# Kernel tuning notes

Hardware: AMD Instinct MI355X
Metric: run time of the kernel (lower is better)

The kernel has to match this reference:

```python
import jax, jax.numpy as jnp
import numpy as np

K = 20
NEG_SLOPE = 0.2
BN_EPS = 1e-5


def knn_idx(x, k):
    # x: (B, C, N) -> neighbor indices (B, N, k) by largest negative sq-distance
    xt = jnp.swapaxes(x, 1, 2)                      # (B, N, C)
    inner = 2.0 * jnp.einsum('bic,bjc->bij', xt, xt)
    sq = jnp.sum(xt * xt, axis=-1)                  # (B, N)
    dist = inner - sq[:, :, None] - sq[:, None, :]  # -||xi-xj||^2
    _, idx = jax.lax.top_k(dist, k)
    return idx


def edge_feature(x, src, idx):
    # x: (B, C, N) centers; src: (B, C, M) gather source; idx: (B, N, k)
    xt = jnp.swapaxes(x, 1, 2)                      # (B, N, C)
    st = jnp.swapaxes(src, 1, 2)                    # (B, M, C)
    b = jnp.arange(xt.shape[0])[:, None, None]
    neigh = st[b, idx]                              # (B, N, k, C)
    center = xt[:, :, None, :]                      # (B, N, 1, C)
    feat = jnp.concatenate(
        [neigh - center, jnp.broadcast_to(center, neigh.shape)], axis=-1)
    return jnp.transpose(feat, (0, 3, 1, 2))        # (B, 2C, N, k)


def conv_bn_lrelu(x, w, gamma, beta):
    # 1x1 conv (no bias) + training-mode BatchNorm2d + LeakyReLU(0.2)
    y = jnp.einsum('oc,bcnk->bonk', w, x)
    mean = jnp.mean(y, axis=(0, 2, 3), keepdims=True)
    var = jnp.var(y, axis=(0, 2, 3), keepdims=True)
    y = (y - mean) * jax.lax.rsqrt(var + BN_EPS)
    y = y * gamma[None, :, None, None] + beta[None, :, None, None]
    return jnp.where(y >= 0, y, NEG_SLOPE * y)


def knn_ia_idx(x, y, k):
    # cosine-similarity KNN from x (B,Cx,N) into y (B,Cy,M), normalize over channels
    xn = x / jnp.maximum(jnp.linalg.norm(x, axis=1, keepdims=True), 1e-12)
    yn = y / jnp.maximum(jnp.linalg.norm(y, axis=1, keepdims=True), 1e-12)
    simi = jnp.einsum('bci,bcj->bij', xn, yn)       # (B, N, M)
    _, idx = jax.lax.top_k(simi, k)
    return idx


def setup_inputs() -> dict:
    key = jax.random.key(0)
    ks = jax.random.split(key, 8)
    B, N, M, EMB = 8, 1024, 1024, 512
    x = jax.random.normal(ks[0], (B, 3, N), dtype=jnp.float32)
    y = jax.random.normal(ks[1], (B, 128, M), dtype=jnp.float32)
    def w(k_, o, c):
        return jax.random.normal(k_, (o, c), dtype=jnp.float32) * (1.0 / np.sqrt(c))
    inp = {
        'x': x, 'y': y,
        'w1': w(ks[2], 64, 6),
        'w2': w(ks[3], 64, 128),
        'w3': w(ks[4], 128, 128),
        'w4': w(ks[5], 256, 256),
        'w5': w(ks[6], EMB, 512),
        'g1': jnp.ones(64), 'b1': jnp.zeros(64),
        'g2': jnp.ones(64), 'b2': jnp.zeros(64),
        'g3': jnp.ones(128), 'b3': jnp.zeros(128),
        'g4': jnp.ones(256), 'b4': jnp.zeros(256),
        'g5': jnp.ones(EMB), 'b5': jnp.zeros(EMB),
    }
    return inp


def reference(x, y, w1, w2, w3, w4, w5, g1, b1, g2, b2, g3, b3, g4, b4, g5, b5):
    # block 1
    h = conv_bn_lrelu(edge_feature(x, x, knn_idx(x, K)), w1, g1, b1)
    x1 = jnp.max(h, axis=-1)                        # (B, 64, N)
    # block 2
    h = conv_bn_lrelu(edge_feature(x1, x1, knn_idx(x1, K)), w2, g2, b2)
    x2 = jnp.max(h, axis=-1)                        # (B, 64, N)
    # block 3
    h = conv_bn_lrelu(edge_feature(x2, x2, knn_idx(x2, K)), w3, g3, b3)
    x3 = jnp.max(h, axis=-1)                        # (B, 128, N)
    # block 4: cross-attention KNN into y (cosine similarity)
    h = conv_bn_lrelu(edge_feature(x3, y, knn_ia_idx(x3, y, K)), w4, g4, b4)
    x4 = jnp.max(h, axis=-1)                        # (B, 256, N)
    # final 1x1 conv + BN + LeakyReLU on concatenated features (512 ch)
    cat = jnp.concatenate([x1, x2, x3, x4], axis=1)  # (B, 512, N)
    out = conv_bn_lrelu(cat[..., None], w5, g5, b5)[..., 0]
    return out                                       # (B, n_emb_dims, N)
```

## Files before the change

kernel.cpp:

```cpp
#include <hip/hip_runtime.h>
#include <hip/hip_bf16.h>

#define KNN 20
#define NEG_SLOPE 0.2f

constexpr int BB = 8;
constexpr int NN = 1024;
constexpr int MM = 1024;

typedef short bf16x8 __attribute__((ext_vector_type(8)));
typedef float f32x4 __attribute__((ext_vector_type(4)));

__device__ __forceinline__ void topk_exact_f64(double (&v)[16], int lane, int* op) {
  for (int r = 0; r < KNN; ++r) {
    double bv = -INFINITY;
    int bj = MM;
#pragma unroll
    for (int m = 0; m < 16; ++m) {
      if (v[m] > bv) { bv = v[m]; bj = m * 64 + lane; }
    }
#pragma unroll
    for (int off = 32; off > 0; off >>= 1) {
      double ov = __shfl_xor(bv, off, 64);
      int oj = __shfl_xor(bj, off, 64);
      if (ov > bv || (ov == bv && oj < bj)) { bv = ov; bj = oj; }
    }
    if (bj < MM && lane == (bj & 63)) v[bj >> 6] = -INFINITY;
    if (lane == 0) op[r] = bj;
  }
}

__device__ __forceinline__ void topk20(double (&v)[16], int lane, int* op) {
  unsigned s[16];
#pragma unroll
  for (int m = 0; m < 16; ++m) {
    float f = (float)v[m];
    unsigned u = __float_as_uint(f);
    u = (u & 0x80000000u) ? ~u : (u | 0x80000000u);
    s[m] = (u & ~1023u) | (unsigned)(1023 - (m * 64 + lane));
  }
#pragma unroll
  for (int p = 1; p < 16; p <<= 1) {
#pragma unroll
    for (int k = p; k >= 1; k >>= 1) {
#pragma unroll
      for (int j = k % p; j + k < 16; j += 2 * k) {
#pragma unroll
        for (int i = 0; i < k; ++i) {
          int a = j + i, b = j + i + k;
          if (b < 16 && (a / (2 * p)) == (b / (2 * p))) {
            unsigned hi = s[a] > s[b] ? s[a] : s[b];
            unsigned lo = s[a] > s[b] ? s[b] : s[a];
            s[a] = hi;
            s[b] = lo;
          }
        }
      }
    }
  }
  unsigned prev = 0;
#pragma unroll
  for (int r = 0; r < KNN; ++r) {
    unsigned win = s[0];
#pragma unroll
    for (int off = 32; off > 0; off >>= 1) {
      unsigned o = __shfl_xor(win, off, 64);
      win = o > win ? o : win;
    }
    if (lane == 0) op[r] = 1023 - (int)(win & 1023u);
    if (s[0] == win) {
#pragma unroll
      for (int i = 0; i < 15; ++i) s[i] = s[i + 1];
      s[15] = 0u;
    }
    prev = win;
  }
  unsigned win21 = s[0];
#pragma unroll
  for (int off = 32; off > 0; off >>= 1) {
    unsigned o = __shfl_xor(win21, off, 64);
    win21 = o > win21 ? o : win21;
  }
  if ((prev >> 10) == (win21 >> 10)) {
    topk_exact_f64(v, lane, op);
  }
}

__global__ __launch_bounds__(256) void k_transpose(
    const float* __restrict__ in, float* __restrict__ out, int C, int Np) {
  int total = BB * C * Np;
  for (int t = blockIdx.x * 256 + threadIdx.x; t < total; t += gridDim.x * 256) {
    int c = t % C;
    int n = (t / C) % Np;
    int b = t / (C * Np);
    out[t] = in[((size_t)b * C + c) * Np + n];
  }
}

__global__ __launch_bounds__(256) void k_cvt_bf16(
    const float* __restrict__ in, __hip_bfloat16* __restrict__ out, int n) {
  int i = blockIdx.x * 256 + threadIdx.x;
  if (i < n) out[i] = __float2bfloat16(in[i]);
}

template <int RECIP>
__global__ __launch_bounds__(256) void k_rowsq(
    const float* __restrict__ A, int ld, int C, double* __restrict__ sq) {
  int p = blockIdx.x * 256 + threadIdx.x;
  if (p >= BB * NN) return;
  const float* row = A + (size_t)p * ld;
  double s = 0.0;
  for (int c = 0; c < C; ++c) { double v = (double)row[c]; s += v * v; }
  if (RECIP) {
    sq[p] = 1.0 / fmax(sqrt(s), 1e-12);
  } else {
    sq[p] = s;
  }
}

__global__ __launch_bounds__(256) void k_knn3(
    const float* __restrict__ xs3, const double* __restrict__ sq, int* __restrict__ idx) {
  __shared__ float P[NN * 3];
  int b = blockIdx.x;
  const float* Xb = xs3 + (size_t)b * NN * 3;
  int tid = threadIdx.x;
  for (int t = tid; t < NN * 3; t += 256) P[t] = Xb[t];
  __syncthreads();
  int wave = tid >> 6, lane = tid & 63;
  int i = blockIdx.y * 4 + wave;
  double xi = (double)P[i * 3], yi = (double)P[i * 3 + 1], zi = (double)P[i * 3 + 2];
  double sqi = sq[b * NN + i];
  double v[16];
#pragma unroll
  for (int m = 0; m < 16; ++m) {
    int j = m * 64 + lane;
    double d = fma(xi, (double)P[j * 3], 0.0);
    d = fma(yi, (double)P[j * 3 + 1], d);
    d = fma(zi, (double)P[j * 3 + 2], d);
    v[m] = 2.0 * d - sqi - sq[b * NN + j];
  }
  int* op = idx + ((size_t)b * NN + i) * KNN;
  topk20(v, lane, op);
}

template <int MODE>
__global__ __launch_bounds__(256) void k_gram2(
    const float* __restrict__ A, int lda, const float* __restrict__ Bm, int ldb,
    const double* __restrict__ sqA, const double* __restrict__ sqB,
    double* __restrict__ D, int C, int b0) {
  __shared__ double As[16][136];
  __shared__ double Bs[16][72];
  int bg = b0 + blockIdx.x;
  int bl = blockIdx.x;
  int j0 = blockIdx.y * 64;
  int i0 = blockIdx.z * 128;
  const float* Ab = A + (size_t)bg * NN * lda;
  const float* Bb = Bm + (size_t)bg * MM * ldb;
  int tx = threadIdx.x, ty = threadIdx.y;
  int tid = ty * 16 + tx;
  double acc[8][4] = {};
  for (int c0 = 0; c0 < C; c0 += 16) {
    for (int r = 0; r < 2; ++r) {
      int li = tid + r * 256;
      int row = li >> 2;
      int f = (li & 3) * 4;
      float4 av = *(const float4*)&Ab[(size_t)(i0 + row) * lda + c0 + f];
      As[f + 0][row] = (double)av.x;
      As[f + 1][row] = (double)av.y;
      As[f + 2][row] = (double)av.z;
      As[f + 3][row] = (double)av.w;
    }
    {
      int row = tid >> 2;
      int f = (tid & 3) * 4;
      float4 bv = *(const float4*)&Bb[(size_t)(j0 + row) * ldb + c0 + f];
      Bs[f + 0][row] = (double)bv.x;
      Bs[f + 1][row] = (double)bv.y;
      Bs[f + 2][row] = (double)bv.z;
      Bs[f + 3][row] = (double)bv.w;
    }
    __syncthreads();
#pragma unroll
    for (int k = 0; k < 16; ++k) {
      double a_[8], b_[4];
#pragma unroll
      for (int ii = 0; ii < 8; ++ii) a_[ii] = As[k][ty * 8 + ii];
#pragma unroll
      for (int jj = 0; jj < 4; ++jj) b_[jj] = Bs[k][jj * 16 + tx];
#pragma unroll
      for (int ii = 0; ii < 8; ++ii)
#pragma unroll
        for (int jj = 0; jj < 4; ++jj)
          acc[ii][jj] = fma(a_[ii], b_[jj], acc[ii][jj]);
    }
    __syncthreads();
  }
  for (int ii = 0; ii < 8; ++ii) {
    int i = i0 + ty * 8 + ii;
    for (int jj = 0; jj < 4; ++jj) {
      int j = j0 + jj * 16 + tx;
      double r = acc[ii][jj];
      if (MODE == 1) r = 2.0 * r - sqA[bg * NN + i] - sqB[bg * NN + j];
      if (MODE == 2) r = r * sqA[bg * NN + i] * sqB[bg * NN + j];
      D[((size_t)bl * NN + i) * MM + j] = r;
    }
  }
}

__global__ __launch_bounds__(256) void k_gram_sym(
    const float* __restrict__ A, int lda, const double* __restrict__ sqA,
    double* __restrict__ D, int C, int b0) {
  __shared__ double As[16][68];
  __shared__ double Bs[16][68];
  __shared__ double T[64][65];
  int p = blockIdx.y;
  int r = (int)((sqrtf(8.f * p + 1.f) - 1.f) * 0.5f);
  while ((r + 1) * (r + 2) / 2 <= p) ++r;
  while (r * (r + 1) / 2 > p) --r;
  int cc = p - r * (r + 1) / 2;
  int i0 = r * 64, j0 = cc * 64;
  int bg = b0 + blockIdx.x;
  int bl = blockIdx.x;
  const float* Ab = A + (size_t)bg * NN * lda;
  int tx = threadIdx.x, ty = threadIdx.y;
  int tid = ty * 16 + tx;
  double acc[4][4] = {};
  for (int c0 = 0; c0 < C; c0 += 16) {
    for (int rr = 0; rr < 4; ++rr) {
      int li = tid + rr * 256;
      int row = li >> 4, k = li & 15;
      int c = c0 + k;
      As[k][row] = (c < C) ? (double)Ab[(size_t)(i0 + row) * lda + c] : 0.0;
      Bs[k][row] = (c < C) ? (double)Ab[(size_t)(j0 + row) * lda + c] : 0.0;
    }
    __syncthreads();
#pragma unroll
    for (int k = 0; k < 16; ++k) {
      double a_[4], b_[4];
#pragma unroll
      for (int ii = 0; ii < 4; ++ii) a_[ii] = As[k][ty * 4 + ii];
#pragma unroll
      for (int jj = 0; jj < 4; ++jj) b_[jj] = Bs[k][jj * 16 + tx];
#pragma unroll
      for (int ii = 0; ii < 4; ++ii)
#pragma unroll
        for (int jj = 0; jj < 4; ++jj)
          acc[ii][jj] = fma(a_[ii], b_[jj], acc[ii][jj]);
    }
    __syncthreads();
  }
  for (int ii = 0; ii < 4; ++ii) {
    int i = i0 + ty * 4 + ii;
    for (int jj = 0; jj < 4; ++jj) {
      int j = j0 + jj * 16 + tx;
      double v = 2.0 * acc[ii][jj] - sqA[bg * NN + i] - sqA[bg * NN + j];
      D[((size_t)bl * NN + i) * MM + j] = v;
      T[jj * 16 + tx][ty * 4 + ii] = v;
    }
  }
  if (i0 != j0) {
    __syncthreads();
    for (int rr = 0; rr < 16; ++rr) {
      int li = tid + rr * 256;
      int jrow = li >> 6, il = li & 63;
      D[((size_t)bl * NN + j0 + jrow) * MM + i0 + il] = T[jrow][il];
    }
  }
}

__global__ __launch_bounds__(256) void k_topk(const double* __restrict__ D,
                                              int* __restrict__ idx, int b0) {
  int wave = threadIdx.x >> 6;
  int lane = threadIdx.x & 63;
  int bl = blockIdx.x;
  int row = blockIdx.y * 4 + wave;
  const double* rp = D + ((size_t)bl * NN + row) * MM;
  double v[16];
#pragma unroll
  for (int m = 0; m < 16; ++m) v[m] = rp[m * 64 + lane];
  int* op = idx + ((size_t)(b0 + bl) * NN + row) * KNN;
  topk20(v, lane, op);
}

__global__ __launch_bounds__(256) void k_featmm(
    const float* __restrict__ src, int lds_, const float* __restrict__ w, int CW,
    float* __restrict__ out, int C, int O, int mode, int Np) {
  __shared__ float As[16][68];
  __shared__ float Ws[16][68];
  int b = blockIdx.x;
  int o0 = blockIdx.y * 64;
  int j0 = blockIdx.z * 64;
  int tx = threadIdx.x, ty = threadIdx.y;
  int tid = ty * 16 + tx;
  const float* Sb = src + (size_t)b * Np * lds_;
  float acc[4][4] = {};
  for (int c0 = 0; c0 < C; c0 += 16) {
    for (int r = 0; r < 4; ++r) {
      int li = tid + r * 256;
      int row = li >> 4, k = li & 15;
      int c = c0 + k;
      As[k][row] = (c < C) ? Sb[(size_t)(j0 + row) * lds_ + c] : 0.f;
      float wv = 0.f;
      if (c < C) {
        const float* wr = w + (size_t)(o0 + row) * CW;
        wv = mode == 0 ? wr[c] : (wr[C + c] - wr[c]);
      }
      Ws[k][row] = wv;
    }
    __syncthreads();
#pragma unroll
    for (int k = 0; k < 16; ++k) {
      float a_[4], b_[4];
#pragma unroll
      for (int ii = 0; ii < 4; ++ii) a_[ii] = As[k][ty * 4 + ii];
#pragma unroll
      for (int jj = 0; jj < 4; ++jj) b_[jj] = Ws[k][tx * 4 + jj];
#pragma unroll
      for (int ii = 0; ii < 4; ++ii)
#pragma unroll
        for (int jj = 0; jj < 4; ++jj)
          acc[ii][jj] = fmaf(a_[ii], b_[jj], acc[ii][jj]);
    }
    __syncthreads();
  }
  for (int ii = 0; ii < 4; ++ii) {
    int j = j0 + ty * 4 + ii;
    float4 v;
    float* vp = &v.x;
    for (int jj = 0; jj < 4; ++jj) vp[jj] = acc[ii][jj];
    *(float4*)&out[((size_t)b * Np + j) * O + o0 + tx * 4] = v;
  }
}

__global__ __launch_bounds__(256) void k_gemm5_mfma(
    const __hip_bfloat16* __restrict__ cath, const __hip_bfloat16* __restrict__ w5h,
    float* __restrict__ out) {
  int b = blockIdx.x;
  int j0 = blockIdx.y * 16;
  int o0 = blockIdx.z * 64 + (threadIdx.x >> 6) * 16;
  int lane = threadIdx.x & 63;
  int m = lane & 15;
  int quad = lane >> 4;
  const __hip_bfloat16* arow = cath + ((size_t)b * NN + j0 + m) * 512 + quad * 8;
  const __hip_bfloat16* brow = w5h + (size_t)(o0 + m) * 512 + quad * 8;
  f32x4 acc = {0.f, 0.f, 0.f, 0.f};
#pragma unroll
  for (int c0 = 0; c0 < 512; c0 += 32) {
    bf16x8 a = *(const bf16x8*)(arow + c0);
    bf16x8 bb = *(const bf16x8*)(brow + c0);
    acc = __builtin_amdgcn_mfma_f32_16x16x32_bf16(a, bb, acc, 0, 0, 0);
  }
  float* obase = &out[((size_t)b * NN + j0 + quad * 4) * 512 + o0 + m];
#pragma unroll
  for (int r = 0; r < 4; ++r) obase[(size_t)r * 512] = acc[r];
}

__global__ __launch_bounds__(256) void k_gather(
    const float* __restrict__ u, const float* __restrict__ t, const int* __restrict__ idx,
    double* __restrict__ stats, float* __restrict__ mx, int O, int srcNp) {
  __shared__ int lidx[16 * KNN];
  __shared__ double rs[256];
  __shared__ double rq[256];
  int b = blockIdx.x;
  int n0 = blockIdx.y * 16;
  int o0 = blockIdx.z * 64;
  int tid = threadIdx.x;
  int lane = tid & 63, nsl = tid >> 6;
  for (int w = tid; w < 16 * KNN; w += 256)
    lidx[w] = idx[((size_t)b * NN + n0) * KNN + w];
  __syncthreads();
  int oo = o0 + lane;
  double s1 = 0.0, s2 = 0.0;
  for (int ns = nsl; ns < 16; ns += 4) {
    size_t row = (size_t)b * NN + n0 + ns;
    float tv = t[row * O + oo];
    float mxv = -INFINITY, a1 = 0.f, a2 = 0.f;
#pragma unroll
    for (int k = 0; k < KNN; ++k) {
      int j = lidx[ns * KNN + k];
      float yv = u[((size_t)b * srcNp + j) * O + oo] + tv;
      mxv = fmaxf(mxv, yv);
      a1 += yv;
      a2 = fmaf(yv, yv, a2);
    }
    mx[row * O + oo] = mxv;
    s1 += (double)a1;
    s2 += (double)a2;
  }
  rs[tid] = s1;
  rq[tid] = s2;
  __syncthreads();
  if (tid < 64) {
    s1 = rs[tid] + rs[tid + 64] + rs[tid + 128] + rs[tid + 192];
    s2 = rq[tid] + rq[tid + 64] + rq[tid + 128] + rq[tid + 192];
    atomicAdd(&stats[o0 + tid], s1);
    atomicAdd(&stats[O + o0 + tid], s2);
  }
}

__global__ void k_bnfin(const double* __restrict__ stats, const float* __restrict__ gamma,
                        const float* __restrict__ beta, float* __restrict__ sc,
                        int O, double cnt) {
  int o = threadIdx.x;
  if (o >= O) return;
  double mean = stats[o] / cnt;
  double var = stats[O + o] / cnt - mean * mean;
  if (var < 0.0) var = 0.0;
  double rstd = 1.0 / sqrt(var + 1e-5);
  float s = gamma[o] * (float)rstd;
  float c = beta[o] - (float)mean * s;
  sc[o] = s;
  sc[O + o] = c;
}

__global__ __launch_bounds__(256) void k_bnapply(
    const float* __restrict__ mx, const float* __restrict__ u, const float* __restrict__ t,
    const int* __restrict__ idx, const float* __restrict__ sc, float* __restrict__ cat,
    __hip_bfloat16* __restrict__ cath, int coff, int O, int srcNp) {
  int i = blockIdx.x * 256 + threadIdx.x;
  int total = BB * NN * O;
  if (i >= total) return;
  int oo = i % O;
  int n = (i / O) % NN;
  int b = i / (O * NN);
  float s = sc[oo], c = sc[O + oo];
  float v;
  if (s >= 0.f) {
    v = mx[i];
  } else {
    float tv = t[i];
    float mn = INFINITY;
    for (int k = 0; k < KNN; ++k) {
      int j = idx[((size_t)b * NN + n) * KNN + k];
      mn = fminf(mn, u[((size_t)b * srcNp + j) * O + oo] + tv);
    }
    v = mn;
  }
  float a = s * v + c;
  a = (a >= 0.f) ? a : NEG_SLOPE * a;
  size_t oidx = ((size_t)b * NN + n) * 512 + coff + oo;
  cat[oidx] = a;
  cath[oidx] = __float2bfloat16(a);
}

__global__ __launch_bounds__(256) void k_stats512(
    const float* __restrict__ y5, double* __restrict__ stats) {
  int b = blockIdx.y;
  int n0 = blockIdx.x * 32;
  int tid = threadIdx.x;
  for (int part = 0; part < 2; ++part) {
    int oo = tid + part * 256;
    float a1 = 0.f, a2 = 0.f;
    for (int ns = 0; ns < 32; ++ns) {
      float v = y5[((size_t)b * NN + n0 + ns) * 512 + oo];
      a1 += v;
      a2 = fmaf(v, v, a2);
    }
    atomicAdd(&stats[oo], (double)a1);
    atomicAdd(&stats[512 + oo], (double)a2);
  }
}

__global__ __launch_bounds__(256) void k_final5b(
    const float* __restrict__ y5, const float* __restrict__ sc, float* __restrict__ out) {
  __shared__ float tile[64][65];
  int b = blockIdx.z;
  int n0 = blockIdx.x * 64;
  int o0 = blockIdx.y * 64;
  int tid = threadIdx.x;
  for (int r = 0; r < 16; ++r) {
    int li = tid + r * 256;
    int nl = li >> 6, ol = li & 63;
    float v = y5[((size_t)b * NN + n0 + nl) * 512 + o0 + ol];
    float a = sc[o0 + ol] * v + sc[512 + o0 + ol];
    a = (a >= 0.f) ? a : NEG_SLOPE * a;
    tile[nl][ol] = a;
  }
  __syncthreads();
  for (int r = 0; r < 16; ++r) {
    int li = tid + r * 256;
    int ol = li >> 6, nl = li & 63;
    out[((size_t)b * 512 + o0 + ol) * NN + n0 + nl] = tile[nl][ol];
  }
}

__global__ __launch_bounds__(256) void k_mmstats(
    const float* __restrict__ src, const float* __restrict__ w,
    double* __restrict__ stats) {
  __shared__ float As[16][68];
  __shared__ float Ws[16][68];
  __shared__ float redS[16][64];
  __shared__ float redQ[16][64];
  int b = blockIdx.z;
  int j0 = blockIdx.y * 64;
  int o0 = blockIdx.x * 64;
  int tx = threadIdx.x, ty = threadIdx.y;
  int tid = ty * 16 + tx;
  const float* Sb = src + (size_t)b * NN * 512;
  float acc[4][4] = {};
  for (int c0 = 0; c0 < 512; c0 += 16) {
    for (int r = 0; r < 4; ++r) {
      int li = tid + r * 256;
      int row = li >> 4, k = li & 15;
      As[k][row] = Sb[(size_t)(j0 + row) * 512 + c0 + k];
      Ws[k][row] = w[(size_t)(o0 + row) * 512 + c0 + k];
    }
    __syncthreads();
#pragma unroll
    for (int k = 0; k < 16; ++k) {
      float a_[4], b_[4];
#pragma unroll
      for (int ii = 0; ii < 4; ++ii) a_[ii] = As[k][ty * 4 + ii];
#pragma unroll
      for (int jj = 0; jj < 4; ++jj) b_[jj] = Ws[k][tx * 4 + jj];
#pragma unroll
      for (int ii = 0; ii < 4; ++ii)
#pragma unroll
        for (int jj = 0; jj < 4; ++jj)
          acc[ii][jj] = fmaf(a_[ii], b_[jj], acc[ii][jj]);
    }
    __syncthreads();
  }
  for (int jj = 0; jj < 4; ++jj) {
    float s = 0.f, q = 0.f;
    for (int ii = 0; ii < 4; ++ii) { float v = acc[ii][jj]; s += v; q += v * v; }
    redS[ty][tx * 4 + jj] = s;
    redQ[ty][tx * 4 + jj] = q;
  }
  __syncthreads();
  if (tid < 64) {
    float s = 0.f, q = 0.f;
    for (int r = 0; r < 16; ++r) { s += redS[r][tid]; q += redQ[r][tid]; }
    atomicAdd(&stats[o0 + tid], (double)s);
    atomicAdd(&stats[512 + o0 + tid], (double)q);
  }
}

__global__ __launch_bounds__(256) void k_final5(
    const float* __restrict__ src, const float* __restrict__ w,
    const float* __restrict__ sc, float* __restrict__ out) {
  __shared__ float As[16][68];
  __shared__ float Ws[16][68];
  __shared__ float tile[64][65];
  int b = blockIdx.z;
  int j0 = blockIdx.y * 64;
  int o0 = blockIdx.x * 64;
  int tx = threadIdx.x, ty = threadIdx.y;
  int tid = ty * 16 + tx;
  const float* Sb = src + (size_t)b * NN * 512;
  float acc[4][4] = {};
  for (int c0 = 0; c0 < 512; c0 += 16) {
    for (int r = 0; r < 4; ++r) {
      int li = tid + r * 256;
      int row = li >> 4, k = li & 15;
      As[k][row] = Sb[(size_t)(j0 + row) * 512 + c0 + k];
      Ws[k][row] = w[(size_t)(o0 + row) * 512 + c0 + k];
    }
    __syncthreads();
#pragma unroll
    for (int k = 0; k < 16; ++k) {
      float a_[4], b_[4];
#pragma unroll
      for (int ii = 0; ii < 4; ++ii) a_[ii] = As[k][ty * 4 + ii];
#pragma unroll
      for (int jj = 0; jj < 4; ++jj) b_[jj] = Ws[k][tx * 4 + jj];
#pragma unroll
      for (int ii = 0; ii < 4; ++ii)
#pragma unroll
        for (int jj = 0; jj < 4; ++jj)
          acc[ii][jj] = fmaf(a_[ii], b_[jj], acc[ii][jj]);
    }
    __syncthreads();
  }
  for (int ii = 0; ii < 4; ++ii)
    for (int jj = 0; jj < 4; ++jj) {
      int nl = ty * 4 + ii, ol = tx * 4 + jj;
      float a = sc[o0 + ol] * acc[ii][jj] + sc[512 + o0 + ol];
      a = (a >= 0.f) ? a : NEG_SLOPE * a;
      tile[nl][ol] = a;
    }
  __syncthreads();
  for (int r = 0; r < 16; ++r) {
    int li = tid + r * 256;
    int ol = li >> 6, nl = li & 63;
    out[((size_t)b * 512 + o0 + ol) * NN + j0 + nl] = tile[nl][ol];
  }
}

extern "C" void kernel_launch(void* const* d_in, const int* in_sizes, int n_in,
                              void* d_out, int out_size, void* d_ws, size_t ws_size,
                              hipStream_t stream) {
  const float* x = (const float*)d_in[0];
  const float* y = (const float*)d_in[1];
  const float* w1 = (const float*)d_in[2];
  const float* w2 = (const float*)d_in[3];
  const float* w3 = (const float*)d_in[4];
  const float* w4 = (const float*)d_in[5];
  const float* w5 = (const float*)d_in[6];
  const float* g1 = (const float*)d_in[7];
  const float* b1 = (const float*)d_in[8];
  const float* g2 = (const float*)d_in[9];
  const float* b2 = (const float*)d_in[10];
  const float* g3 = (const float*)d_in[11];
  const float* b3 = (const float*)d_in[12];
  const float* g4 = (const float*)d_in[13];
  const float* b4 = (const float*)d_in[14];
  const float* g5 = (const float*)d_in[15];
  const float* b5 = (const float*)d_in[16];

  char* base = (char*)d_ws;
  size_t off = 0;
  auto alloc = [&](size_t bytes) -> char* {
    char* p = base + off;
    off += (bytes + 255) & ~(size_t)255;
    return p;
  };
  double* st = (double*)alloc(1024 * 8);
  float* sc  = (float*)alloc(1024 * 4);
  double* sq  = (double*)alloc((size_t)BB * NN * 8);
  double* rnx = (double*)alloc((size_t)BB * NN * 8);
  double* rny = (double*)alloc((size_t)BB * MM * 8);
  int*   idxb = (int*)alloc((size_t)BB * NN * KNN * 4);
  float* xs3 = (float*)alloc((size_t)BB * NN * 3 * 4);
  float* ys  = (float*)alloc((size_t)BB * MM * 128 * 4);
  float* cat = (float*)alloc((size_t)BB * NN * 512 * 4);
  __hip_bfloat16* cath = (__hip_bfloat16*)alloc((size_t)BB * NN * 512 * 2);
  __hip_bfloat16* w5h  = (__hip_bfloat16*)alloc((size_t)512 * 512 * 2);
  size_t ddBatchBytes = (size_t)NN * MM * 8;
  size_t avail = (ws_size > off) ? (ws_size - off) : 0;
  int CB = (int)(avail / ddBatchBytes);
  if (CB < 1) CB = 1;
  if (CB > BB) CB = BB;
  char*  U   = alloc((size_t)CB * ddBatchBytes);
  double* DD = (double*)U;
  float* tt  = (float*)U;
  float* y5  = (float*)U;
  float* uu  = (float*)d_out;
  float* mx  = (float*)d_out + (size_t)2 * 1024 * 1024;
  float* outp = (float*)d_out;

  const dim3 blk2(16, 16);
  const double cntE = (double)BB * NN * KNN;

  auto knn = [&](const float* A, int lda, const float* Bm, int ldb,
                 const double* sa, const double* sb, int C, int mode, int sym) {
    for (int b0 = 0; b0 < BB; b0 += CB) {
      int cb = (BB - b0 < CB) ? (BB - b0) : CB;
      if (sym) {
        k_gram_sym<<<dim3(cb, 136), blk2, 0, stream>>>(A, lda, sa, DD, C, b0);
      } else {
        dim3 g(cb, MM / 64, NN / 128);
        if (mode == 1) k_gram2<1><<<g, blk2, 0, stream>>>(A, lda, Bm, ldb, sa, sb, DD, C, b0);
        else           k_gram2<2><<<g, blk2, 0, stream>>>(A, lda, Bm, ldb, sa, sb, DD, C, b0);
      }
      k_topk<<<dim3(cb, 256), 256, 0, stream>>>(DD, idxb, b0);
    }
  };

  auto edge_layer = [&](const float* ctr, int ldc, const float* src, int ldsrc, int srcNp,
                        const float* w, int CW, const float* g, const float* bb,
                        int C, int O, int coff) {
    k_featmm<<<dim3(8, O / 64, 16), blk2, 0, stream>>>(src, ldsrc, w, CW, uu, C, O, 0, srcNp);
    k_featmm<<<dim3(8, O / 64, 16), blk2, 0, stream>>>(ctr, ldc, w, CW, tt, C, O, 1, NN);
    hipMemsetAsync(st, 0, 1024 * 8, stream);
    k_gather<<<dim3(BB, NN / 16, O / 64), 256, 0, stream>>>(uu, tt, idxb, st, mx, O, srcNp);
    k_bnfin<<<1, O, 0, stream>>>(st, g, bb, sc, O, cntE);
    k_bnapply<<<(BB * NN * O + 255) / 256, 256, 0, stream>>>(mx, uu, tt, idxb, sc, cat,
                                                             cath, coff, O, srcNp);
  };

  k_transpose<<<96, 256, 0, stream>>>(x, xs3, 3, NN);
  k_transpose<<<2048, 256, 0, stream>>>(y, ys, 128, MM);
  k_cvt_bf16<<<1024, 256, 0, stream>>>(w5, w5h, 512 * 512);

  k_rowsq<0><<<32, 256, 0, stream>>>(xs3, 3, 3, sq);
  k_knn3<<<dim3(BB, 256), 256, 0, stream>>>(xs3, sq, idxb);
  edge_layer(xs3, 3, xs3, 3, NN, w1, 6, g1, b1, 3, 64, 0);

  k_rowsq<0><<<32, 256, 0, stream>>>(cat, 512, 64, sq);
  knn(cat, 512, cat, 512, sq, sq, 64, 1, 1);
  edge_layer(cat, 512, cat, 512, NN, w2, 128, g2, b2, 64, 64, 64);

  k_rowsq<0><<<32, 256, 0, stream>>>(cat + 64, 512, 64, sq);
  knn(cat + 64, 512, cat + 64, 512, sq, sq, 64, 1, 1);
  edge_layer(cat + 64, 512, cat + 64, 512, NN, w3, 128, g3, b3, 64, 128, 128);

  k_rowsq<1><<<32, 256, 0, stream>>>(cat + 128, 512, 128, rnx);
  k_rowsq<1><<<32, 256, 0, stream>>>(ys, 128, 128, rny);
  knn(cat + 128, 512, ys, 128, rnx, rny, 128, 2, 0);
  edge_layer(cat + 128, 512, ys, 128, MM, w4, 256, g4, b4, 128, 256, 256);

  hipMemsetAsync(st, 0, 1024 * 8, stream);
  if (CB >= 2) {
    k_gemm5_mfma<<<dim3(BB, 64, 8), 256, 0, stream>>>(cath, w5h, y5);
    k_stats512<<<dim3(32, 8), 256, 0, stream>>>(y5, st);
    k_bnfin<<<1, 512, 0, stream>>>(st, g5, b5, sc, 512, (double)(BB * NN));
    k_final5b<<<dim3(16, 8, 8), 256, 0, stream>>>(y5, sc, outp);
  } else {
    k_mmstats<<<dim3(8, 16, 8), blk2, 0, stream>>>(cat, w5, st);
    k_bnfin<<<1, 512, 0, stream>>>(st, g5, b5, sc, 512, (double)(BB * NN));
    k_final5<<<dim3(8, 16, 8), blk2, 0, stream>>>(cat, w5, sc, outp);
  }
}
```

Baseline: 694.9 us.

## Emit packed 32-bit top-k keys from gram kernels and merge feature matmuls

```diff
diff --git a/kernel.cpp b/kernel.cpp
--- a/kernel.cpp
+++ b/kernel.cpp
@@ -10,6 +10,13 @@
 
 typedef short bf16x8 __attribute__((ext_vector_type(8)));
 typedef float f32x4 __attribute__((ext_vector_type(4)));
+
+__device__ __forceinline__ unsigned pack_key(double d, int j) {
+  float f = (float)d;
+  unsigned u = __float_as_uint(f);
+  u = (u & 0x80000000u) ? ~u : (u | 0x80000000u);
+  return (u & ~1023u) | (unsigned)(1023 - j);
+}
 
 __device__ __forceinline__ void topk_exact_f64(double (&v)[16], int lane, int* op) {
   for (int r = 0; r < KNN; ++r) {
@@ -30,15 +37,7 @@
   }
 }
 
-__device__ __forceinline__ void topk20(double (&v)[16], int lane, int* op) {
-  unsigned s[16];
-#pragma unroll
-  for (int m = 0; m < 16; ++m) {
-    float f = (float)v[m];
-    unsigned u = __float_as_uint(f);
-    u = (u & 0x80000000u) ? ~u : (u | 0x80000000u);
-    s[m] = (u & ~1023u) | (unsigned)(1023 - (m * 64 + lane));
-  }
+__device__ __forceinline__ bool topk20_fast(unsigned (&s)[16], int lane, int* op) {
 #pragma unroll
   for (int p = 1; p < 16; p <<= 1) {
 #pragma unroll
@@ -81,9 +80,7 @@
     unsigned o = __shfl_xor(win21, off, 64);
     win21 = o > win21 ? o : win21;
   }
-  if ((prev >> 10) == (win21 >> 10)) {
-    topk_exact_f64(v, lane, op);
-  }
+  return (prev >> 10) == (win21 >> 10);
 }
 
 __global__ __launch_bounds__(256) void k_transpose(
@@ -131,6 +128,7 @@
   double xi = (double)P[i * 3], yi = (double)P[i * 3 + 1], zi = (double)P[i * 3 + 2];
   double sqi = sq[b * NN + i];
   double v[16];
+  unsigned s[16];
 #pragma unroll
   for (int m = 0; m < 16; ++m) {
     int j = m * 64 + lane;
@@ -138,18 +136,19 @@
     d = fma(yi, (double)P[j * 3 + 1], d);
     d = fma(zi, (double)P[j * 3 + 2], d);
     v[m] = 2.0 * d - sqi - sq[b * NN + j];
+    s[m] = pack_key(v[m], j);
   }
   int* op = idx + ((size_t)b * NN + i) * KNN;
-  topk20(v, lane, op);
+  if (topk20_fast(s, lane, op)) topk_exact_f64(v, lane, op);
 }
 
 template <int MODE>
 __global__ __launch_bounds__(256) void k_gram2(
     const float* __restrict__ A, int lda, const float* __restrict__ Bm, int ldb,
     const double* __restrict__ sqA, const double* __restrict__ sqB,
-    double* __restrict__ D, int C, int b0) {
-  __shared__ double As[16][136];
-  __shared__ double Bs[16][72];
+    double* __restrict__ D, unsigned* __restrict__ kk, int C, int b0) {
+  __shared__ double As[16][137];
+  __shared__ double Bs[16][73];
   int bg = b0 + blockIdx.x;
   int bl = blockIdx.x;
   int j0 = blockIdx.y * 64;
@@ -202,16 +201,18 @@
       double r = acc[ii][jj];
       if (MODE == 1) r = 2.0 * r - sqA[bg * NN + i] - sqB[bg * NN + j];
       if (MODE == 2) r = r * sqA[bg * NN + i] * sqB[bg * NN + j];
-      D[((size_t)bl * NN + i) * MM + j] = r;
+      size_t o = ((size_t)bl * NN + i) * MM + j;
+      D[o] = r;
+      kk[o] = pack_key(r, j);
     }
   }
 }
 
 __global__ __launch_bounds__(256) void k_gram_sym(
     const float* __restrict__ A, int lda, const double* __restrict__ sqA,
-    double* __restrict__ D, int C, int b0) {
-  __shared__ double As[16][68];
-  __shared__ double Bs[16][68];
+    double* __restrict__ D, unsigned* __restrict__ kk, int C, int b0) {
+  __shared__ double As[16][69];
+  __shared__ double Bs[16][69];
   __shared__ double T[64][65];
   int p = blockIdx.y;
   int r = (int)((sqrtf(8.f * p + 1.f) - 1.f) * 0.5f);
@@ -254,7 +255,9 @@
     for (int jj = 0; jj < 4; ++jj) {
       int j = j0 + jj * 16 + tx;
       double v = 2.0 * acc[ii][jj] - sqA[bg * NN + i] - sqA[bg * NN + j];
-      D[((size_t)bl * NN + i) * MM + j] = v;
+      size_t o = ((size_t)bl * NN + i) * MM + j;
+      D[o] = v;
+      kk[o] = pack_key(v, j);
       T[jj * 16 + tx][ty * 4 + ii] = v;
     }
   }
@@ -263,33 +266,51 @@
     for (int rr = 0; rr < 16; ++rr) {
       int li = tid + rr * 256;
       int jrow = li >> 6, il = li & 63;
-      D[((size_t)bl * NN + j0 + jrow) * MM + i0 + il] = T[jrow][il];
-    }
-  }
-}
-
-__global__ __launch_bounds__(256) void k_topk(const double* __restrict__ D,
+      double v = T[jrow][il];
+      size_t o = ((size_t)bl * NN + j0 + jrow) * MM + i0 + il;
+      D[o] = v;
+      kk[o] = pack_key(v, i0 + il);
+    }
+  }
+}
+
+__global__ __launch_bounds__(256) void k_topk(const unsigned* __restrict__ kk,
+                                              const double* __restrict__ D,
                                               int* __restrict__ idx, int b0) {
   int wave = threadIdx.x >> 6;
   int lane = threadIdx.x & 63;
   int bl = blockIdx.x;
   int row = blockIdx.y * 4 + wave;
-  const double* rp = D + ((size_t)bl * NN + row) * MM;
-  double v[16];
-#pragma unroll
-  for (int m = 0; m < 16; ++m) v[m] = rp[m * 64 + lane];
+  const unsigned* rp = kk + ((size_t)bl * NN + row) * MM;
+  unsigned s[16];
+#pragma unroll
+  for (int m = 0; m < 16; ++m) s[m] = rp[m * 64 + lane];
   int* op = idx + ((size_t)(b0 + bl) * NN + row) * KNN;
-  topk20(v, lane, op);
-}
-
-__global__ __launch_bounds__(256) void k_featmm(
-    const float* __restrict__ src, int lds_, const float* __restrict__ w, int CW,
-    float* __restrict__ out, int C, int O, int mode, int Np) {
+  if (topk20_fast(s, lane, op)) {
+    const double* dp = D + ((size_t)bl * NN + row) * MM;
+    double v[16];
+#pragma unroll
+    for (int m = 0; m < 16; ++m) v[m] = dp[m * 64 + lane];
+    topk_exact_f64(v, lane, op);
+  }
+}
+
+__global__ __launch_bounds__(256) void k_featmm2(
+    const float* __restrict__ src0, int ld0, int Np0,
+    const float* __restrict__ src1, int ld1,
+    const float* __restrict__ w, int CW,
+    float* __restrict__ out0, float* __restrict__ out1, int C, int O) {
   __shared__ float As[16][68];
   __shared__ float Ws[16][68];
+  int nbo = O >> 6;
   int b = blockIdx.x;
-  int o0 = blockIdx.y * 64;
+  int mode = blockIdx.y >= nbo;
+  int o0 = (blockIdx.y - (mode ? nbo : 0)) * 64;
   int j0 = blockIdx.z * 64;
+  const float* src = mode ? src1 : src0;
+  int lds_ = mode ? ld1 : ld0;
+  int Np = mode ? NN : Np0;
+  float* out = mode ? out1 : out0;
   int tx = threadIdx.x, ty = threadIdx.y;
   int tid = ty * 16 + tx;
   const float* Sb = src + (size_t)b * Np * lds_;
@@ -627,11 +648,13 @@
   __hip_bfloat16* cath = (__hip_bfloat16*)alloc((size_t)BB * NN * 512 * 2);
   __hip_bfloat16* w5h  = (__hip_bfloat16*)alloc((size_t)512 * 512 * 2);
   size_t ddBatchBytes = (size_t)NN * MM * 8;
+  size_t kkBatchBytes = (size_t)NN * MM * 4;
   size_t avail = (ws_size > off) ? (ws_size - off) : 0;
-  int CB = (int)(avail / ddBatchBytes);
+  int CB = (int)(avail / (ddBatchBytes + kkBatchBytes));
   if (CB < 1) CB = 1;
   if (CB > BB) CB = BB;
   char*  U   = alloc((size_t)CB * ddBatchBytes);
+  unsigned* KK = (unsigned*)alloc((size_t)CB * kkBatchBytes);
   double* DD = (double*)U;
   float* tt  = (float*)U;
   float* y5  = (float*)U;
@@ -647,21 +670,23 @@
     for (int b0 = 0; b0 < BB; b0 += CB) {
       int cb = (BB - b0 < CB) ? (BB - b0) : CB;
       if (sym) {
-        k_gram_sym<<<dim3(cb, 136), blk2, 0, stream>>>(A, lda, sa, DD, C, b0);
+        k_gram_sym<<<dim3(cb, 136), blk2, 0, stream>>>(A, lda, sa, DD, KK, C, b0);
       } else {
         dim3 g(cb, MM / 64, NN / 128);
-        if (mode == 1) k_gram2<1><<<g, blk2, 0, stream>>>(A, lda, Bm, ldb, sa, sb, DD, C, b0);
-        else           k_gram2<2><<<g, blk2, 0, stream>>>(A, lda, Bm, ldb, sa, sb, DD, C, b0);
+        if (mode == 1)
+          k_gram2<1><<<g, blk2, 0, stream>>>(A, lda, Bm, ldb, sa, sb, DD, KK, C, b0);
+        else
+          k_gram2<2><<<g, blk2, 0, stream>>>(A, lda, Bm, ldb, sa, sb, DD, KK, C, b0);
       }
-      k_topk<<<dim3(cb, 256), 256, 0, stream>>>(DD, idxb, b0);
+      k_topk<<<dim3(cb, 256), 256, 0, stream>>>(KK, DD, idxb, b0);
     }
   };
 
   auto edge_layer = [&](const float* ctr, int ldc, const float* src, int ldsrc, int srcNp,
                         const float* w, int CW, const float* g, const float* bb,
                         int C, int O, int coff) {
-    k_featmm<<<dim3(8, O / 64, 16), blk2, 0, stream>>>(src, ldsrc, w, CW, uu, C, O, 0, srcNp);
-    k_featmm<<<dim3(8, O / 64, 16), blk2, 0, stream>>>(ctr, ldc, w, CW, tt, C, O, 1, NN);
+    k_featmm2<<<dim3(8, 2 * (O / 64), 16), blk2, 0, stream>>>(src, ldsrc, srcNp, ctr, ldc,
+                                                              w, CW, uu, tt, C, O);
     hipMemsetAsync(st, 0, 1024 * 8, stream);
     k_gather<<<dim3(BB, NN / 16, O / 64), 256, 0, stream>>>(uu, tt, idxb, st, mx, O, srcNp);
     k_bnfin<<<1, O, 0, stream>>>(st, g, bb, sc, O, cntE);
```

New measurement: 676.0 us. 2.7% less time.
